# Performance work log

Measured on AMD Instinct MI355X. Metric: run time of the kernel, lower is better.

Reference implementation:

```python
import jax, jax.numpy as jnp
import numpy as np

HEADS = 16

def setup_inputs() -> dict:
    key = jax.random.key(0)
    k1, k2, k3 = jax.random.split(key, 3)
    B, T, C = 4, 2048, 1024
    s = 0.02
    return {
        "x": jax.random.normal(k1, (B, T, C), dtype=jnp.float32),
        "W_qkv": jax.random.normal(k2, (C, 3 * C), dtype=jnp.float32) * s,
        "b_qkv": jnp.zeros((3 * C,), dtype=jnp.float32),
        "W_pr": jax.random.normal(k3, (C, C), dtype=jnp.float32) * s,
        "b_pr": jnp.zeros((C,), dtype=jnp.float32),
    }

def reference(x, W_qkv, b_qkv, W_pr, b_pr):
    B, T, C = x.shape
    H = HEADS
    hd = C // H
    qkv = x @ W_qkv + b_qkv                     # [B,T,3C]
    q, k, v = jnp.split(qkv, 3, axis=-1)
    # [B,T,C] -> [B,H,T,hd]
    q = q.reshape(B, T, H, hd).transpose(0, 2, 1, 3)
    k = k.reshape(B, T, H, hd).transpose(0, 2, 1, 3)
    v = v.reshape(B, T, H, hd).transpose(0, 2, 1, 3)
    att = jnp.einsum('bhqd,bhkd->bhqk', q, k) * (1.0 / jnp.sqrt(jnp.float32(hd)))
    causal = jnp.tril(jnp.ones((T, T), dtype=bool))
    att = jnp.where(causal[None, None, :, :], att, jnp.float32(-jnp.inf))
    att = jax.nn.softmax(att, axis=-1)
    y = jnp.einsum('bhqk,bhkd->bhqd', att, v)   # [B,H,T,hd]
    y = y.transpose(0, 2, 1, 3).reshape(B, T, C)  # merge heads
    return y @ W_pr + b_pr
```

## Files before the change

kernel.cpp:

```cpp
#include <hip/hip_runtime.h>


typedef __attribute__((ext_vector_type(8))) short bf16x8;
typedef __attribute__((ext_vector_type(4))) float f32x4;

#define MFMA16(a, b, c) __builtin_amdgcn_mfma_f32_16x16x32_bf16(a, b, c, 0, 0, 0)

#define QK_SCALE 0.1803368801111244f

__device__ __forceinline__ unsigned short f2bf(float f) {
    union { float f; unsigned u; } v; v.f = f;
    unsigned r = v.u + 0x7fffu + ((v.u >> 16) & 1u);
    return (unsigned short)(r >> 16);
}

typedef __attribute__((address_space(1))) const unsigned int guint;
typedef __attribute__((address_space(3))) unsigned int luint;
__device__ __forceinline__ void gload16(const void* g, void* l) {
    __builtin_amdgcn_global_load_lds((guint*)g, (luint*)l, 16, 0, 0);
}

__device__ __forceinline__ float exp2_hw(float x) {
    float y;
    asm("v_exp_f32 %0, %1" : "=v"(y) : "v"(x));
    return y;
}

__device__ __forceinline__ unsigned cvt_pk_bf16(float lo, float hi) {
    unsigned w;
    asm("v_cvt_pk_bf16_f32 %0, %1, %2" : "=v"(w) : "v"(lo), "v"(hi));
    return w;
}

__global__ __launch_bounds__(256) void k_conv(const float* __restrict__ in,
                                              unsigned short* __restrict__ out,
                                              int n4) {
    int i = blockIdx.x * 256 + threadIdx.x;
    if (i >= n4) return;
    float4 v = reinterpret_cast<const float4*>(in)[i];
    ushort4 o;
    o.x = f2bf(v.x); o.y = f2bf(v.y); o.z = f2bf(v.z); o.w = f2bf(v.w);
    reinterpret_cast<ushort4*>(out)[i] = o;
}

__global__ __launch_bounds__(256) void k_transpose_conv(const float* __restrict__ W,
                                                        unsigned short* __restrict__ Wt,
                                                        int K, int N) {
    __shared__ unsigned short tile[32][33];
    int tx = threadIdx.x & 31, ty = threadIdx.x >> 5;
    int bn = blockIdx.x * 32, bk = blockIdx.y * 32;
#pragma unroll
    for (int i = 0; i < 32; i += 8)
        tile[ty + i][tx] = f2bf(W[(size_t)(bk + ty + i) * N + bn + tx]);
    __syncthreads();
#pragma unroll
    for (int i = 0; i < 32; i += 8)
        Wt[(size_t)(bn + ty + i) * K + bk + tx] = tile[tx][ty + i];
}

__device__ __forceinline__ int swz_src_col(int off) {
    return ((((off >> 4) & 3) ^ ((off >> 7) & 3)) << 3);
}

__global__ __launch_bounds__(256) void k_gemm_qkv(
    const unsigned short* __restrict__ A,
    const unsigned short* __restrict__ Bt,
    const float* __restrict__ bias,
    unsigned short* __restrict__ Qo,
    unsigned short* __restrict__ Ko,
    unsigned short* __restrict__ Vto)
{
    constexpr int K = 1024;
    __shared__ alignas(16) char smem[33280];
    unsigned short* Ep = (unsigned short*)smem;
    const int tid = threadIdx.x;
    const int wave = tid >> 6, lane = tid & 63;
    const int wr = wave >> 1, wc = wave & 1;
    const int lrow = lane & 15, lkg = lane >> 4;
    const int bm = blockIdx.y * 128, bn = blockIdx.x * 128;

    const int off0 = tid * 16, off1 = off0 + 4096;
    const unsigned short* gA0 = A + (size_t)(bm + (off0 >> 6)) * K + swz_src_col(off0);
    const unsigned short* gA1 = A + (size_t)(bm + (off1 >> 6)) * K + swz_src_col(off1);
    const unsigned short* gB0 = Bt + (size_t)(bn + (off0 >> 6)) * K + swz_src_col(off0);
    const unsigned short* gB1 = Bt + (size_t)(bn + (off1 >> 6)) * K + swz_src_col(off1);

    f32x4 acc[4][4] = {};

#define GSTAGE(kt_, bufn_)                                          \
    do {                                                            \
        char* ba_ = smem + (bufn_) * 16384;                         \
        gload16(gA0 + (kt_), ba_ + off0);                           \
        gload16(gA1 + (kt_), ba_ + off1);                           \
        gload16(gB0 + (kt_), ba_ + 8192 + off0);                    \
        gload16(gB1 + (kt_), ba_ + 8192 + off1);                    \
    } while (0)

    GSTAGE(0, 0);
    int buf = 0;
    for (int t = 0; t < 32; ++t) {
        if (t < 31) {
            GSTAGE((t + 1) * 32, buf ^ 1);
            asm volatile("s_waitcnt vmcnt(4)" ::: "memory");
        } else {
            asm volatile("s_waitcnt vmcnt(0)" ::: "memory");
        }
        __builtin_amdgcn_s_barrier();
        __builtin_amdgcn_sched_barrier(0);

        const char* Asb = smem + buf * 16384;
        const char* Bsb = Asb + 8192;
        bf16x8 af[4], bfr[4];
#pragma unroll
        for (int m = 0; m < 4; ++m) {
            int R = wr * 64 + m * 16 + lrow;
            af[m] = *reinterpret_cast<const bf16x8*>(
                Asb + R * 64 + ((lkg ^ ((R >> 1) & 3)) << 4));
        }
#pragma unroll
        for (int n = 0; n < 4; ++n) {
            int R = wc * 64 + n * 16 + lrow;
            bfr[n] = *reinterpret_cast<const bf16x8*>(
                Bsb + R * 64 + ((lkg ^ ((R >> 1) & 3)) << 4));
        }
        __builtin_amdgcn_s_setprio(1);
#pragma unroll
        for (int m = 0; m < 4; ++m)
#pragma unroll
            for (int n = 0; n < 4; ++n)
                acc[m][n] = MFMA16(af[m], bfr[n], acc[m][n]);
        __builtin_amdgcn_s_setprio(0);
        __builtin_amdgcn_s_barrier();
        buf ^= 1;
    }
#undef GSTAGE

    const int which = bn >> 10;
    const int h0 = (bn & 1023) >> 6;
    const int bq = bm >> 11;
    const int t0 = bm & 2047;
    const float qs = (which == 0) ? QK_SCALE : 1.0f;

#pragma unroll
    for (int m = 0; m < 4; ++m) {
        int rl = wr * 64 + m * 16 + lkg * 4;
#pragma unroll
        for (int n = 0; n < 4; ++n) {
            int cl = wc * 64 + n * 16 + lrow;
            float bia = bias[bn + cl];
#pragma unroll
            for (int r = 0; r < 4; ++r) {
                unsigned short val = f2bf((acc[m][n][r] + bia) * qs);
                if (which == 2) {
                    int tl = rl + r;
                    int pt = (tl & 0x60) | ((tl & 15) << 1) | ((tl >> 4) & 1);
                    Ep[cl * 130 + pt] = val;
                } else {
                    Ep[(rl + r) * 130 + cl] = val;
                }
            }
        }
    }
    __syncthreads();

    const int chunk = tid & 15, rbase = tid >> 4;
    if (which != 2) {
        const int head = chunk >> 3, d0 = (chunk & 7) * 8;
        unsigned short* dst = (which == 0 ? Qo : Ko) +
            (size_t)((bq * 16 + h0 + head) * 2048 + t0) * 64 + d0;
#pragma unroll
        for (int s = 0; s < 8; ++s) {
            int row = s * 16 + rbase;
            bf16x8 v = *reinterpret_cast<const bf16x8*>(&Ep[row * 130 + chunk * 8]);
            *reinterpret_cast<bf16x8*>(dst + (size_t)row * 64) = v;
        }
    } else {
#pragma unroll
        for (int s = 0; s < 8; ++s) {
            int pd = s * 16 + rbase;
            bf16x8 v = *reinterpret_cast<const bf16x8*>(&Ep[pd * 130 + chunk * 8]);
            int bh = bq * 16 + h0 + (pd >> 6);
            size_t addr = ((size_t)(bh * 64 + (pd & 63)) * 2048) + t0 + chunk * 8;
            *reinterpret_cast<bf16x8*>(Vto + addr) = v;
        }
    }
}

__global__ __launch_bounds__(256, 2) void k_attn(
    const unsigned short* __restrict__ Q,
    const unsigned short* __restrict__ Kg,
    const unsigned short* __restrict__ Vt,
    unsigned short* __restrict__ Y)
{
    __shared__ alignas(16) unsigned short Ks[2][4096];
    __shared__ alignas(16) unsigned short Vs[2][4096];
    __shared__ unsigned int Pu[4][32][36];
    const int tid = threadIdx.x;
    const int wave = tid >> 6, lane = tid & 63;
    const int lrow = lane & 15, lkg = lane >> 4;
    const int bh = blockIdx.x & 63;
    const int s = (blockIdx.x >> 6) & 3;
    const int band = blockIdx.x >> 8;
    const int j = (band == 0) ? 15 - s : (band == 1) ? 8 + s : (band == 2) ? 7 - s : s;
    const int qt = 4 * j + wave;
    const int q0 = qt * 32;
    const int nt = 2 * j + 2;
    const int b = bh >> 4, hh = bh & 15;

    const unsigned short* Qh = Q + (size_t)bh * 2048 * 64;
    const unsigned short* Kh = Kg + (size_t)bh * 2048 * 64;
    const unsigned short* Vh = Vt + (size_t)bh * 64 * 2048;

    const int srow = tid >> 3;
    const int swz = ((tid & 7) ^ (srow & 7)) << 3;
    const unsigned short* gK = Kh + (size_t)srow * 64 + swz;
    const unsigned short* gV = Vh + (size_t)srow * 2048 + swz;
    char* dK0 = (char*)&Ks[0][0] + tid * 16;
    char* dV0 = (char*)&Vs[0][0] + tid * 16;

    bf16x8 aq[2][2];
#pragma unroll
    for (int h = 0; h < 2; ++h)
#pragma unroll
        for (int ks = 0; ks < 2; ++ks)
            aq[h][ks] = *reinterpret_cast<const bf16x8*>(
                &Qh[(size_t)(q0 + h * 16 + lrow) * 64 + ks * 32 + lkg * 8]);

    f32x4 acc[2][4] = {};
    float lsum[2][4] = {};

#define STAGE(kb_, bufn_)                                           \
    do {                                                            \
        const unsigned short* k0_ = gK + (kb_) * 64;                \
        const unsigned short* v0_ = gV + (kb_);                     \
        char* dk_ = dK0 + (bufn_) * 8192;                           \
        char* dv_ = dV0 + (bufn_) * 8192;                           \
        gload16(k0_, dk_);                                          \
        gload16(k0_ + 2048, dk_ + 4096);                            \
        gload16(v0_, dv_);                                          \
        gload16(v0_ + 65536, dv_ + 4096);                           \
    } while (0)

    STAGE(0, 0);
    int buf = 0;

    for (int t = 0; t < nt; ++t) {
        if (t + 1 < nt) {
            STAGE((t + 1) * 64, buf ^ 1);
            asm volatile("s_waitcnt vmcnt(4)" ::: "memory");
        } else {
            asm volatile("s_waitcnt vmcnt(0)" ::: "memory");
        }
        __builtin_amdgcn_s_barrier();
        __builtin_amdgcn_sched_barrier(0);

        const int kb = t * 64;
        const char* kbase = (const char*)&Ks[buf][0];
        const char* vbase = (const char*)&Vs[buf][0];

        f32x4 s_[2][4] = {};
        __builtin_amdgcn_s_setprio(1);
#pragma unroll
        for (int sub = 0; sub < 4; ++sub) {
            int krow = sub * 16 + lrow;
            bf16x8 kf0 = *reinterpret_cast<const bf16x8*>(
                kbase + krow * 128 + ((lkg ^ (krow & 7)) << 4));
            bf16x8 kf1 = *reinterpret_cast<const bf16x8*>(
                kbase + krow * 128 + (((4 + lkg) ^ (krow & 7)) << 4));
            s_[0][sub] = MFMA16(aq[0][0], kf0, s_[0][sub]);
            s_[0][sub] = MFMA16(aq[0][1], kf1, s_[0][sub]);
            s_[1][sub] = MFMA16(aq[1][0], kf0, s_[1][sub]);
            s_[1][sub] = MFMA16(aq[1][1], kf1, s_[1][sub]);
        }
        __builtin_amdgcn_s_setprio(0);

        const bool need_mask = (kb + 64 > q0);
#pragma unroll
        for (int h = 0; h < 2; ++h)
#pragma unroll
            for (int sub = 0; sub < 4; ++sub)
#pragma unroll
                for (int r = 0; r < 4; ++r) {
                    float v = s_[h][sub][r];
                    if (need_mask) {
                        int key = kb + sub * 16 + lrow;
                        int q = q0 + h * 16 + lkg * 4 + r;
                        v = (key <= q) ? v : -1e30f;
                    }
                    s_[h][sub][r] = exp2_hw(v);
                }

#pragma unroll
        for (int h = 0; h < 2; ++h) {
            int prow = h * 16 + lkg * 4;
#pragma unroll
            for (int r = 0; r < 4; ++r) {
                lsum[h][r] += (s_[h][0][r] + s_[h][1][r]) + (s_[h][2][r] + s_[h][3][r]);
                Pu[wave][prow + r][lrow]      = cvt_pk_bf16(s_[h][0][r], s_[h][1][r]);
                Pu[wave][prow + r][16 + lrow] = cvt_pk_bf16(s_[h][2][r], s_[h][3][r]);
            }
        }

        bf16x8 pf[2][2];
#pragma unroll
        for (int h = 0; h < 2; ++h)
#pragma unroll
            for (int kc = 0; kc < 2; ++kc)
                pf[h][kc] = *reinterpret_cast<const bf16x8*>(
                    &Pu[wave][h * 16 + lrow][kc * 16 + lkg * 4]);

        __builtin_amdgcn_s_setprio(1);
#pragma unroll
        for (int tt = 0; tt < 4; ++tt) {
            int vrow = tt * 16 + lrow;
            bf16x8 vf0 = *reinterpret_cast<const bf16x8*>(
                vbase + vrow * 128 + ((lkg ^ (vrow & 7)) << 4));
            bf16x8 vf1 = *reinterpret_cast<const bf16x8*>(
                vbase + vrow * 128 + (((4 + lkg) ^ (vrow & 7)) << 4));
            acc[0][tt] = MFMA16(pf[0][0], vf0, acc[0][tt]);
            acc[0][tt] = MFMA16(pf[0][1], vf1, acc[0][tt]);
            acc[1][tt] = MFMA16(pf[1][0], vf0, acc[1][tt]);
            acc[1][tt] = MFMA16(pf[1][1], vf1, acc[1][tt]);
        }
        __builtin_amdgcn_s_setprio(0);

        __builtin_amdgcn_s_barrier();
        buf ^= 1;
    }
#undef STAGE

#pragma unroll
    for (int h = 0; h < 2; ++h) {
        float inv[4];
#pragma unroll
        for (int r = 0; r < 4; ++r) {
            float l = lsum[h][r];
            l += __shfl_xor(l, 1); l += __shfl_xor(l, 2);
            l += __shfl_xor(l, 4); l += __shfl_xor(l, 8);
            inv[r] = 1.0f / l;
        }
#pragma unroll
        for (int t = 0; t < 4; ++t)
#pragma unroll
            for (int r = 0; r < 4; ++r) {
                int q = q0 + h * 16 + lkg * 4 + r;
                size_t idx = ((size_t)b * 2048 + q) * 1024 + hh * 64 + t * 16 + lrow;
                Y[idx] = f2bf(acc[h][t][r] * inv[r]);
            }
    }
}

__global__ __launch_bounds__(256) void k_gemm_proj(
    const unsigned short* __restrict__ A,
    const unsigned short* __restrict__ Bt,
    const float* __restrict__ bias,
    float* __restrict__ out)
{
    constexpr int K = 1024;
    __shared__ alignas(16) char smem[33024];
    float* Ep2 = (float*)smem;
    const int tid = threadIdx.x;
    const int wave = tid >> 6, lane = tid & 63;
    const int wr = wave >> 1, wc = wave & 1;
    const int lrow = lane & 15, lkg = lane >> 4;
    const int bm = blockIdx.y * 128, bn = blockIdx.x * 128;

    const int off0 = tid * 16, off1 = off0 + 4096;
    const unsigned short* gA0 = A + (size_t)(bm + (off0 >> 6)) * K + swz_src_col(off0);
    const unsigned short* gA1 = A + (size_t)(bm + (off1 >> 6)) * K + swz_src_col(off1);
    const unsigned short* gB0 = Bt + (size_t)(bn + (off0 >> 6)) * K + swz_src_col(off0);
    const unsigned short* gB1 = Bt + (size_t)(bn + (off1 >> 6)) * K + swz_src_col(off1);

    f32x4 acc[4][4] = {};

#define GSTAGE(kt_, bufn_)                                          \
    do {                                                            \
        char* ba_ = smem + (bufn_) * 16384;                         \
        gload16(gA0 + (kt_), ba_ + off0);                           \
        gload16(gA1 + (kt_), ba_ + off1);                           \
        gload16(gB0 + (kt_), ba_ + 8192 + off0);                    \
        gload16(gB1 + (kt_), ba_ + 8192 + off1);                    \
    } while (0)

    GSTAGE(0, 0);
    int buf = 0;
    for (int t = 0; t < 32; ++t) {
        if (t < 31) {
            GSTAGE((t + 1) * 32, buf ^ 1);
            asm volatile("s_waitcnt vmcnt(4)" ::: "memory");
        } else {
            asm volatile("s_waitcnt vmcnt(0)" ::: "memory");
        }
        __builtin_amdgcn_s_barrier();
        __builtin_amdgcn_sched_barrier(0);

        const char* Asb = smem + buf * 16384;
        const char* Bsb = Asb + 8192;
        bf16x8 af[4], bfr[4];
#pragma unroll
        for (int m = 0; m < 4; ++m) {
            int R = wr * 64 + m * 16 + lrow;
            af[m] = *reinterpret_cast<const bf16x8*>(
                Asb + R * 64 + ((lkg ^ ((R >> 1) & 3)) << 4));
        }
#pragma unroll
        for (int n = 0; n < 4; ++n) {
            int R = wc * 64 + n * 16 + lrow;
            bfr[n] = *reinterpret_cast<const bf16x8*>(
                Bsb + R * 64 + ((lkg ^ ((R >> 1) & 3)) << 4));
        }
        __builtin_amdgcn_s_setprio(1);
#pragma unroll
        for (int m = 0; m < 4; ++m)
#pragma unroll
            for (int n = 0; n < 4; ++n)
                acc[m][n] = MFMA16(af[m], bfr[n], acc[m][n]);
        __builtin_amdgcn_s_setprio(0);
        __builtin_amdgcn_s_barrier();
        buf ^= 1;
    }
#undef GSTAGE

    const int chunk = tid >> 3;
    const int r8 = tid & 7;
#pragma unroll
    for (int p = 0; p < 2; ++p) {
        __syncthreads();
        if (wr == p) {
#pragma unroll
            for (int m = 0; m < 4; ++m)
#pragma unroll
                for (int n = 0; n < 4; ++n) {
                    int cl = wc * 64 + n * 16 + lrow;
                    float bia = bias[bn + cl];
#pragma unroll
                    for (int r = 0; r < 4; ++r)
                        Ep2[(m * 16 + lkg * 4 + r) * 129 + cl] = acc[m][n][r] + bia;
                }
        }
        __syncthreads();
#pragma unroll
        for (int s = 0; s < 8; ++s) {
            int row = r8 * 8 + s;
            float4 v = *reinterpret_cast<const float4*>(&Ep2[row * 129 + chunk * 4]);
            *reinterpret_cast<float4*>(&out[(size_t)(bm + p * 64 + row) * 1024 + bn + chunk * 4]) = v;
        }
    }
}

extern "C" void kernel_launch(void* const* d_in, const int* in_sizes, int n_in,
                              void* d_out, int out_size, void* d_ws, size_t ws_size,
                              hipStream_t stream) {
    const float* x    = (const float*)d_in[0];
    const float* Wqkv = (const float*)d_in[1];
    const float* bqkv = (const float*)d_in[2];
    const float* Wpr  = (const float*)d_in[3];
    const float* bpr  = (const float*)d_in[4];
    float* out = (float*)d_out;

    char* ws = (char*)d_ws;
    unsigned short* xb  = (unsigned short*)(ws);
    unsigned short* Wqt = (unsigned short*)(ws + 16777216);
    unsigned short* Wpt = (unsigned short*)(ws + 23068672);
    unsigned short* Qb  = (unsigned short*)(ws + 25165824);
    unsigned short* Kb  = (unsigned short*)(ws + 41943040);
    unsigned short* Vt  = (unsigned short*)(ws + 58720256);
    unsigned short* Y   = xb;

    k_conv<<<8192, 256, 0, stream>>>(x, xb, 8388608 / 4);
    k_transpose_conv<<<dim3(96, 32), 256, 0, stream>>>(Wqkv, Wqt, 1024, 3072);
    k_transpose_conv<<<dim3(32, 32), 256, 0, stream>>>(Wpr, Wpt, 1024, 1024);
    k_gemm_qkv<<<dim3(24, 64), 256, 0, stream>>>(xb, Wqt, bqkv, Qb, Kb, Vt);
    k_attn<<<1024, 256, 0, stream>>>(Qb, Kb, Vt, Y);
    k_gemm_proj<<<dim3(8, 64), 256, 0, stream>>>(Y, Wpt, bpr, out);
}
```

Baseline: 178.4 us.

## Enlarge GEMM tiles to 256x256 with 512 threads and triple-buffered LDS pipeline

Both the QKV and output-projection GEMMs move from 128x128 tiles with 4 waves to 256x256 tiles with 8 waves, each wave computing 128x64. The LDS staging ring grows from two to three buffers with a prefetch distance of two. The epilogues are split into row halves or quarters so the staging buffer fits in the enlarged shared memory. The aim is more operand reuse per byte loaded and better latency hiding. The cost is much larger LDS per block and far fewer blocks: 384 for QKV and 128 for projection, which may leave CUs idle or create tail imbalance.

```diff
diff --git a/kernel.cpp b/kernel.cpp
--- a/kernel.cpp
+++ b/kernel.cpp
@@ -62,7 +62,7 @@
     return ((((off >> 4) & 3) ^ ((off >> 7) & 3)) << 3);
 }
 
-__global__ __launch_bounds__(256) void k_gemm_qkv(
+__global__ __launch_bounds__(512, 2) void k_gemm_qkv(
     const unsigned short* __restrict__ A,
     const unsigned short* __restrict__ Bt,
     const float* __restrict__ bias,
@@ -71,36 +71,39 @@
     unsigned short* __restrict__ Vto)
 {
     constexpr int K = 1024;
-    __shared__ alignas(16) char smem[33280];
-    unsigned short* Ep = (unsigned short*)smem;
+    __shared__ alignas(16) char smem[98304];
     const int tid = threadIdx.x;
     const int wave = tid >> 6, lane = tid & 63;
-    const int wr = wave >> 1, wc = wave & 1;
+    const int wr = wave >> 2, wc = wave & 3;
     const int lrow = lane & 15, lkg = lane >> 4;
-    const int bm = blockIdx.y * 128, bn = blockIdx.x * 128;
-
-    const int off0 = tid * 16, off1 = off0 + 4096;
+    const int bm = blockIdx.y * 256, bn = blockIdx.x * 256;
+
+    const int off0 = tid * 16, off1 = off0 + 8192;
     const unsigned short* gA0 = A + (size_t)(bm + (off0 >> 6)) * K + swz_src_col(off0);
     const unsigned short* gA1 = A + (size_t)(bm + (off1 >> 6)) * K + swz_src_col(off1);
     const unsigned short* gB0 = Bt + (size_t)(bn + (off0 >> 6)) * K + swz_src_col(off0);
     const unsigned short* gB1 = Bt + (size_t)(bn + (off1 >> 6)) * K + swz_src_col(off1);
 
-    f32x4 acc[4][4] = {};
-
-#define GSTAGE(kt_, bufn_)                                          \
+    f32x4 acc[8][4] = {};
+
+#define GSTAGE(kt_, slot_)                                          \
     do {                                                            \
-        char* ba_ = smem + (bufn_) * 16384;                         \
-        gload16(gA0 + (kt_), ba_ + off0);                           \
-        gload16(gA1 + (kt_), ba_ + off1);                           \
-        gload16(gB0 + (kt_), ba_ + 8192 + off0);                    \
-        gload16(gB1 + (kt_), ba_ + 8192 + off1);                    \
+        char* base_ = smem + (slot_) * 32768;                       \
+        gload16(gA0 + (kt_), base_ + off0);                         \
+        gload16(gA1 + (kt_), base_ + off1);                         \
+        gload16(gB0 + (kt_), base_ + 16384 + off0);                 \
+        gload16(gB1 + (kt_), base_ + 16384 + off1);                 \
     } while (0)
 
     GSTAGE(0, 0);
-    int buf = 0;
+    GSTAGE(32, 1);
+    int cs = 0;
     for (int t = 0; t < 32; ++t) {
-        if (t < 31) {
-            GSTAGE((t + 1) * 32, buf ^ 1);
+        if (t < 30) {
+            int ns = cs + 2; if (ns >= 3) ns -= 3;
+            GSTAGE((t + 2) * 32, ns);
+            asm volatile("s_waitcnt vmcnt(8)" ::: "memory");
+        } else if (t == 30) {
             asm volatile("s_waitcnt vmcnt(4)" ::: "memory");
         } else {
             asm volatile("s_waitcnt vmcnt(0)" ::: "memory");
@@ -108,30 +111,30 @@
         __builtin_amdgcn_s_barrier();
         __builtin_amdgcn_sched_barrier(0);
 
-        const char* Asb = smem + buf * 16384;
-        const char* Bsb = Asb + 8192;
-        bf16x8 af[4], bfr[4];
-#pragma unroll
-        for (int m = 0; m < 4; ++m) {
-            int R = wr * 64 + m * 16 + lrow;
+        const char* Ab = smem + cs * 32768;
+        const char* Bb = Ab + 16384;
+        bf16x8 af[8], bfr[4];
+#pragma unroll
+        for (int m = 0; m < 8; ++m) {
+            int R = wr * 128 + m * 16 + lrow;
             af[m] = *reinterpret_cast<const bf16x8*>(
-                Asb + R * 64 + ((lkg ^ ((R >> 1) & 3)) << 4));
+                Ab + R * 64 + ((lkg ^ ((R >> 1) & 3)) << 4));
         }
 #pragma unroll
         for (int n = 0; n < 4; ++n) {
             int R = wc * 64 + n * 16 + lrow;
             bfr[n] = *reinterpret_cast<const bf16x8*>(
-                Bsb + R * 64 + ((lkg ^ ((R >> 1) & 3)) << 4));
+                Bb + R * 64 + ((lkg ^ ((R >> 1) & 3)) << 4));
         }
         __builtin_amdgcn_s_setprio(1);
 #pragma unroll
-        for (int m = 0; m < 4; ++m)
+        for (int m = 0; m < 8; ++m)
 #pragma unroll
             for (int n = 0; n < 4; ++n)
                 acc[m][n] = MFMA16(af[m], bfr[n], acc[m][n]);
         __builtin_amdgcn_s_setprio(0);
         __builtin_amdgcn_s_barrier();
-        buf ^= 1;
+        ++cs; if (cs == 3) cs = 0;
     }
 #undef GSTAGE
 
@@ -140,48 +143,55 @@
     const int bq = bm >> 11;
     const int t0 = bm & 2047;
     const float qs = (which == 0) ? QK_SCALE : 1.0f;
-
-#pragma unroll
-    for (int m = 0; m < 4; ++m) {
-        int rl = wr * 64 + m * 16 + lkg * 4;
-#pragma unroll
-        for (int n = 0; n < 4; ++n) {
-            int cl = wc * 64 + n * 16 + lrow;
-            float bia = bias[bn + cl];
-#pragma unroll
-            for (int r = 0; r < 4; ++r) {
-                unsigned short val = f2bf((acc[m][n][r] + bia) * qs);
-                if (which == 2) {
-                    int tl = rl + r;
-                    int pt = (tl & 0x60) | ((tl & 15) << 1) | ((tl >> 4) & 1);
-                    Ep[cl * 130 + pt] = val;
-                } else {
-                    Ep[(rl + r) * 130 + cl] = val;
+    unsigned short* Ep = (unsigned short*)smem;
+
+#pragma unroll
+    for (int p = 0; p < 2; ++p) {
+        __syncthreads();
+        if (wr == p) {
+#pragma unroll
+            for (int m = 0; m < 8; ++m) {
+                int tl = m * 16 + lkg * 4;
+#pragma unroll
+                for (int n = 0; n < 4; ++n) {
+                    int cl = wc * 64 + n * 16 + lrow;
+                    float bia = bias[bn + cl];
+#pragma unroll
+                    for (int r = 0; r < 4; ++r) {
+                        unsigned short val = f2bf((acc[m][n][r] + bia) * qs);
+                        int trow = tl + r;
+                        if (which == 2) {
+                            int pt = (trow & 0x60) | ((trow & 15) << 1) | ((trow >> 4) & 1);
+                            Ep[cl * 130 + pt] = val;
+                        } else {
+                            Ep[trow * 258 + cl] = val;
+                        }
+                    }
                 }
             }
         }
-    }
-    __syncthreads();
-
-    const int chunk = tid & 15, rbase = tid >> 4;
-    if (which != 2) {
-        const int head = chunk >> 3, d0 = (chunk & 7) * 8;
-        unsigned short* dst = (which == 0 ? Qo : Ko) +
-            (size_t)((bq * 16 + h0 + head) * 2048 + t0) * 64 + d0;
-#pragma unroll
-        for (int s = 0; s < 8; ++s) {
-            int row = s * 16 + rbase;
-            bf16x8 v = *reinterpret_cast<const bf16x8*>(&Ep[row * 130 + chunk * 8]);
-            *reinterpret_cast<bf16x8*>(dst + (size_t)row * 64) = v;
-        }
-    } else {
-#pragma unroll
-        for (int s = 0; s < 8; ++s) {
-            int pd = s * 16 + rbase;
-            bf16x8 v = *reinterpret_cast<const bf16x8*>(&Ep[pd * 130 + chunk * 8]);
-            int bh = bq * 16 + h0 + (pd >> 6);
-            size_t addr = ((size_t)(bh * 64 + (pd & 63)) * 2048) + t0 + chunk * 8;
-            *reinterpret_cast<bf16x8*>(Vto + addr) = v;
+        __syncthreads();
+        if (which != 2) {
+            const int chunk = tid & 31, rbase = tid >> 5;
+            const int head = h0 + (chunk >> 3), d0 = (chunk & 7) * 8;
+            unsigned short* dst = (which == 0 ? Qo : Ko) +
+                (size_t)((bq * 16 + head) * 2048 + t0 + p * 128) * 64 + d0;
+#pragma unroll
+            for (int s = 0; s < 8; ++s) {
+                int row = s * 16 + rbase;
+                bf16x8 v = *reinterpret_cast<const bf16x8*>(&Ep[row * 258 + chunk * 8]);
+                *reinterpret_cast<bf16x8*>(dst + (size_t)row * 64) = v;
+            }
+        } else {
+            const int chunkt = tid & 15, crow = tid >> 4;
+#pragma unroll
+            for (int s = 0; s < 8; ++s) {
+                int cl = s * 32 + crow;
+                bf16x8 v = *reinterpret_cast<const bf16x8*>(&Ep[cl * 130 + chunkt * 8]);
+                int bh = bq * 16 + h0 + (cl >> 6);
+                size_t addr = ((size_t)(bh * 64 + (cl & 63)) * 2048) + t0 + p * 128 + chunkt * 8;
+                *reinterpret_cast<bf16x8*>(Vto + addr) = v;
+            }
         }
     }
 }
@@ -350,43 +360,46 @@
     }
 }
 
-__global__ __launch_bounds__(256) void k_gemm_proj(
+__global__ __launch_bounds__(512, 2) void k_gemm_proj(
     const unsigned short* __restrict__ A,
     const unsigned short* __restrict__ Bt,
     const float* __restrict__ bias,
     float* __restrict__ out)
 {
     constexpr int K = 1024;
-    __shared__ alignas(16) char smem[33024];
-    float* Ep2 = (float*)smem;
+    __shared__ alignas(16) char smem[98304];
     const int tid = threadIdx.x;
     const int wave = tid >> 6, lane = tid & 63;
-    const int wr = wave >> 1, wc = wave & 1;
+    const int wr = wave >> 2, wc = wave & 3;
     const int lrow = lane & 15, lkg = lane >> 4;
-    const int bm = blockIdx.y * 128, bn = blockIdx.x * 128;
-
-    const int off0 = tid * 16, off1 = off0 + 4096;
+    const int bm = blockIdx.y * 256, bn = blockIdx.x * 256;
+
+    const int off0 = tid * 16, off1 = off0 + 8192;
     const unsigned short* gA0 = A + (size_t)(bm + (off0 >> 6)) * K + swz_src_col(off0);
     const unsigned short* gA1 = A + (size_t)(bm + (off1 >> 6)) * K + swz_src_col(off1);
     const unsigned short* gB0 = Bt + (size_t)(bn + (off0 >> 6)) * K + swz_src_col(off0);
     const unsigned short* gB1 = Bt + (size_t)(bn + (off1 >> 6)) * K + swz_src_col(off1);
 
-    f32x4 acc[4][4] = {};
-
-#define GSTAGE(kt_, bufn_)                                          \
+    f32x4 acc[8][4] = {};
+
+#define GSTAGE(kt_, slot_)                                          \
     do {                                                            \
-        char* ba_ = smem + (bufn_) * 16384;                         \
-        gload16(gA0 + (kt_), ba_ + off0);                           \
-        gload16(gA1 + (kt_), ba_ + off1);                           \
-        gload16(gB0 + (kt_), ba_ + 8192 + off0);                    \
-        gload16(gB1 + (kt_), ba_ + 8192 + off1);                    \
+        char* base_ = smem + (slot_) * 32768;                       \
+        gload16(gA0 + (kt_), base_ + off0);                         \
+        gload16(gA1 + (kt_), base_ + off1);                         \
+        gload16(gB0 + (kt_), base_ + 16384 + off0);                 \
+        gload16(gB1 + (kt_), base_ + 16384 + off1);                 \
     } while (0)
 
     GSTAGE(0, 0);
-    int buf = 0;
+    GSTAGE(32, 1);
+    int cs = 0;
     for (int t = 0; t < 32; ++t) {
-        if (t < 31) {
-            GSTAGE((t + 1) * 32, buf ^ 1);
+        if (t < 30) {
+            int ns = cs + 2; if (ns >= 3) ns -= 3;
+            GSTAGE((t + 2) * 32, ns);
+            asm volatile("s_waitcnt vmcnt(8)" ::: "memory");
+        } else if (t == 30) {
             asm volatile("s_waitcnt vmcnt(4)" ::: "memory");
         } else {
             asm volatile("s_waitcnt vmcnt(0)" ::: "memory");
@@ -394,56 +407,61 @@
         __builtin_amdgcn_s_barrier();
         __builtin_amdgcn_sched_barrier(0);
 
-        const char* Asb = smem + buf * 16384;
-        const char* Bsb = Asb + 8192;
-        bf16x8 af[4], bfr[4];
-#pragma unroll
-        for (int m = 0; m < 4; ++m) {
-            int R = wr * 64 + m * 16 + lrow;
+        const char* Ab = smem + cs * 32768;
+        const char* Bb = Ab + 16384;
+        bf16x8 af[8], bfr[4];
+#pragma unroll
+        for (int m = 0; m < 8; ++m) {
+            int R = wr * 128 + m * 16 + lrow;
             af[m] = *reinterpret_cast<const bf16x8*>(
-                Asb + R * 64 + ((lkg ^ ((R >> 1) & 3)) << 4));
+                Ab + R * 64 + ((lkg ^ ((R >> 1) & 3)) << 4));
         }
 #pragma unroll
         for (int n = 0; n < 4; ++n) {
             int R = wc * 64 + n * 16 + lrow;
             bfr[n] = *reinterpret_cast<const bf16x8*>(
-                Bsb + R * 64 + ((lkg ^ ((R >> 1) & 3)) << 4));
+                Bb + R * 64 + ((lkg ^ ((R >> 1) & 3)) << 4));
         }
         __builtin_amdgcn_s_setprio(1);
 #pragma unroll
-        for (int m = 0; m < 4; ++m)
+        for (int m = 0; m < 8; ++m)
 #pragma unroll
             for (int n = 0; n < 4; ++n)
                 acc[m][n] = MFMA16(af[m], bfr[n], acc[m][n]);
         __builtin_amdgcn_s_setprio(0);
         __builtin_amdgcn_s_barrier();
-        buf ^= 1;
+        ++cs; if (cs == 3) cs = 0;
     }
 #undef GSTAGE
 
-    const int chunk = tid >> 3;
-    const int r8 = tid & 7;
-#pragma unroll
-    for (int p = 0; p < 2; ++p) {
+    float* Ep2 = (float*)smem;
+#pragma unroll
+    for (int p = 0; p < 4; ++p) {
         __syncthreads();
-        if (wr == p) {
-#pragma unroll
-            for (int m = 0; m < 4; ++m)
+        if (wr == (p >> 1)) {
+            int mbase = (p & 1) * 4;
+#pragma unroll
+            for (int mm = 0; mm < 4; ++mm) {
+                int m = mbase + mm;
+                int rl = mm * 16 + lkg * 4;
 #pragma unroll
                 for (int n = 0; n < 4; ++n) {
                     int cl = wc * 64 + n * 16 + lrow;
                     float bia = bias[bn + cl];
 #pragma unroll
                     for (int r = 0; r < 4; ++r)
-                        Ep2[(m * 16 + lkg * 4 + r) * 129 + cl] = acc[m][n][r] + bia;
+                        Ep2[(rl + r) * 257 + cl] = acc[m][n][r] + bia;
                 }
+            }
         }
         __syncthreads();
+        const int chunk = tid & 63, rbase = tid >> 6;
 #pragma unroll
         for (int s = 0; s < 8; ++s) {
-            int row = r8 * 8 + s;
-            float4 v = *reinterpret_cast<const float4*>(&Ep2[row * 129 + chunk * 4]);
-            *reinterpret_cast<float4*>(&out[(size_t)(bm + p * 64 + row) * 1024 + bn + chunk * 4]) = v;
+            int row = s * 8 + rbase;
+            float4 v = *reinterpret_cast<const float4*>(&Ep2[row * 257 + chunk * 4]);
+            *reinterpret_cast<float4*>(
+                &out[(size_t)(bm + p * 64 + row) * 1024 + bn + chunk * 4]) = v;
         }
     }
 }
@@ -470,7 +488,7 @@
     k_conv<<<8192, 256, 0, stream>>>(x, xb, 8388608 / 4);
     k_transpose_conv<<<dim3(96, 32), 256, 0, stream>>>(Wqkv, Wqt, 1024, 3072);
     k_transpose_conv<<<dim3(32, 32), 256, 0, stream>>>(Wpr, Wpt, 1024, 1024);
-    k_gemm_qkv<<<dim3(24, 64), 256, 0, stream>>>(xb, Wqt, bqkv, Qb, Kb, Vt);
+    k_gemm_qkv<<<dim3(12, 32), 512, 0, stream>>>(xb, Wqt, bqkv, Qb, Kb, Vt);
     k_attn<<<1024, 256, 0, stream>>>(Qb, Kb, Vt, Y);
-    k_gemm_proj<<<dim3(8, 64), 256, 0, stream>>>(Y, Wpt, bpr, out);
-}
+    k_gemm_proj<<<dim3(4, 32), 512, 0, stream>>>(Y, Wpt, bpr, out);
+}
```

Result: slower. 208.7 us (+16.9%).

## Enlarge QKV GEMM tile to 256x128 and fuse prep conversions into one launch

Applied to the files above, without the earlier changes.

The QKV projection GEMM now computes 256x128 output tiles (8x4 MFMA accumulators per wave) instead of 128x128, halving the grid and reusing each B tile across twice as many rows. The epilogue is staged through shared memory in two halves to fit the LDS budget. The x conversion and both weight transpose-conversions are merged into a single k_prep launch to cut launch overhead. The larger tile raises register pressure (launch_bounds 256,2) and leaves fewer blocks (768) to fill the CUs.

```diff
diff --git a/kernel.cpp b/kernel.cpp
--- a/kernel.cpp
+++ b/kernel.cpp
@@ -32,23 +32,26 @@
     return w;
 }
 
-__global__ __launch_bounds__(256) void k_conv(const float* __restrict__ in,
-                                              unsigned short* __restrict__ out,
-                                              int n4) {
-    int i = blockIdx.x * 256 + threadIdx.x;
-    if (i >= n4) return;
-    float4 v = reinterpret_cast<const float4*>(in)[i];
-    ushort4 o;
-    o.x = f2bf(v.x); o.y = f2bf(v.y); o.z = f2bf(v.z); o.w = f2bf(v.w);
-    reinterpret_cast<ushort4*>(out)[i] = o;
-}
-
-__global__ __launch_bounds__(256) void k_transpose_conv(const float* __restrict__ W,
-                                                        unsigned short* __restrict__ Wt,
-                                                        int K, int N) {
+__global__ __launch_bounds__(256) void k_prep(
+    const float* __restrict__ x, unsigned short* __restrict__ xb,
+    const float* __restrict__ Wqkv, unsigned short* __restrict__ Wqt,
+    const float* __restrict__ Wpr, unsigned short* __restrict__ Wpt) {
     __shared__ unsigned short tile[32][33];
+    const int b = blockIdx.x;
+    if (b < 8192) {
+        int i = b * 256 + threadIdx.x;
+        float4 v = reinterpret_cast<const float4*>(x)[i];
+        ushort4 o;
+        o.x = f2bf(v.x); o.y = f2bf(v.y); o.z = f2bf(v.z); o.w = f2bf(v.w);
+        reinterpret_cast<ushort4*>(xb)[i] = o;
+        return;
+    }
+    const float* W; unsigned short* Wt; int K, N, idx;
+    if (b < 11264) { W = Wqkv; Wt = Wqt; K = 1024; N = 3072; idx = b - 8192;  }
+    else           { W = Wpr;  Wt = Wpt; K = 1024; N = 1024; idx = b - 11264; }
+    const int nb = N / 32;
+    const int bn = (idx % nb) * 32, bk = (idx / nb) * 32;
     int tx = threadIdx.x & 31, ty = threadIdx.x >> 5;
-    int bn = blockIdx.x * 32, bk = blockIdx.y * 32;
 #pragma unroll
     for (int i = 0; i < 32; i += 8)
         tile[ty + i][tx] = f2bf(W[(size_t)(bk + ty + i) * N + bn + tx]);
@@ -62,7 +65,7 @@
     return ((((off >> 4) & 3) ^ ((off >> 7) & 3)) << 3);
 }
 
-__global__ __launch_bounds__(256) void k_gemm_qkv(
+__global__ __launch_bounds__(256, 2) void k_gemm_qkv(
     const unsigned short* __restrict__ A,
     const unsigned short* __restrict__ Bt,
     const float* __restrict__ bias,
@@ -71,29 +74,37 @@
     unsigned short* __restrict__ Vto)
 {
     constexpr int K = 1024;
-    __shared__ alignas(16) char smem[33280];
-    unsigned short* Ep = (unsigned short*)smem;
+    __shared__ alignas(16) char smem[49152];
     const int tid = threadIdx.x;
     const int wave = tid >> 6, lane = tid & 63;
     const int wr = wave >> 1, wc = wave & 1;
     const int lrow = lane & 15, lkg = lane >> 4;
-    const int bm = blockIdx.y * 128, bn = blockIdx.x * 128;
-
-    const int off0 = tid * 16, off1 = off0 + 4096;
-    const unsigned short* gA0 = A + (size_t)(bm + (off0 >> 6)) * K + swz_src_col(off0);
-    const unsigned short* gA1 = A + (size_t)(bm + (off1 >> 6)) * K + swz_src_col(off1);
-    const unsigned short* gB0 = Bt + (size_t)(bn + (off0 >> 6)) * K + swz_src_col(off0);
-    const unsigned short* gB1 = Bt + (size_t)(bn + (off1 >> 6)) * K + swz_src_col(off1);
-
-    f32x4 acc[4][4] = {};
-
-#define GSTAGE(kt_, bufn_)                                          \
+    const int bm = blockIdx.y * 256, bn = blockIdx.x * 128;
+
+    const unsigned short* gA[4];
+    const unsigned short* gB[2];
+#pragma unroll
+    for (int i = 0; i < 4; ++i) {
+        int off = tid * 16 + i * 4096;
+        gA[i] = A + (size_t)(bm + (off >> 6)) * K + swz_src_col(off);
+    }
+#pragma unroll
+    for (int i = 0; i < 2; ++i) {
+        int off = tid * 16 + i * 4096;
+        gB[i] = Bt + (size_t)(bn + (off >> 6)) * K + swz_src_col(off);
+    }
+
+    f32x4 acc[8][4] = {};
+
+#define GSTAGE(kt_, slot_)                                          \
     do {                                                            \
-        char* ba_ = smem + (bufn_) * 16384;                         \
-        gload16(gA0 + (kt_), ba_ + off0);                           \
-        gload16(gA1 + (kt_), ba_ + off1);                           \
-        gload16(gB0 + (kt_), ba_ + 8192 + off0);                    \
-        gload16(gB1 + (kt_), ba_ + 8192 + off1);                    \
+        char* base_ = smem + (slot_) * 24576;                       \
+        gload16(gA[0] + (kt_), base_ + tid * 16);                   \
+        gload16(gA[1] + (kt_), base_ + 4096 + tid * 16);            \
+        gload16(gA[2] + (kt_), base_ + 8192 + tid * 16);            \
+        gload16(gA[3] + (kt_), base_ + 12288 + tid * 16);           \
+        gload16(gB[0] + (kt_), base_ + 16384 + tid * 16);           \
+        gload16(gB[1] + (kt_), base_ + 20480 + tid * 16);           \
     } while (0)
 
     GSTAGE(0, 0);
@@ -101,31 +112,31 @@
     for (int t = 0; t < 32; ++t) {
         if (t < 31) {
             GSTAGE((t + 1) * 32, buf ^ 1);
-            asm volatile("s_waitcnt vmcnt(4)" ::: "memory");
+            asm volatile("s_waitcnt vmcnt(6)" ::: "memory");
         } else {
             asm volatile("s_waitcnt vmcnt(0)" ::: "memory");
         }
         __builtin_amdgcn_s_barrier();
         __builtin_amdgcn_sched_barrier(0);
 
-        const char* Asb = smem + buf * 16384;
-        const char* Bsb = Asb + 8192;
-        bf16x8 af[4], bfr[4];
-#pragma unroll
-        for (int m = 0; m < 4; ++m) {
-            int R = wr * 64 + m * 16 + lrow;
+        const char* Ab = smem + buf * 24576;
+        const char* Bb = Ab + 16384;
+        bf16x8 af[8], bfr[4];
+#pragma unroll
+        for (int m = 0; m < 8; ++m) {
+            int R = wr * 128 + m * 16 + lrow;
             af[m] = *reinterpret_cast<const bf16x8*>(
-                Asb + R * 64 + ((lkg ^ ((R >> 1) & 3)) << 4));
+                Ab + R * 64 + ((lkg ^ ((R >> 1) & 3)) << 4));
         }
 #pragma unroll
         for (int n = 0; n < 4; ++n) {
             int R = wc * 64 + n * 16 + lrow;
             bfr[n] = *reinterpret_cast<const bf16x8*>(
-                Bsb + R * 64 + ((lkg ^ ((R >> 1) & 3)) << 4));
+                Bb + R * 64 + ((lkg ^ ((R >> 1) & 3)) << 4));
         }
         __builtin_amdgcn_s_setprio(1);
 #pragma unroll
-        for (int m = 0; m < 4; ++m)
+        for (int m = 0; m < 8; ++m)
 #pragma unroll
             for (int n = 0; n < 4; ++n)
                 acc[m][n] = MFMA16(af[m], bfr[n], acc[m][n]);
@@ -140,48 +151,55 @@
     const int bq = bm >> 11;
     const int t0 = bm & 2047;
     const float qs = (which == 0) ? QK_SCALE : 1.0f;
-
-#pragma unroll
-    for (int m = 0; m < 4; ++m) {
-        int rl = wr * 64 + m * 16 + lkg * 4;
-#pragma unroll
-        for (int n = 0; n < 4; ++n) {
-            int cl = wc * 64 + n * 16 + lrow;
-            float bia = bias[bn + cl];
-#pragma unroll
-            for (int r = 0; r < 4; ++r) {
-                unsigned short val = f2bf((acc[m][n][r] + bia) * qs);
-                if (which == 2) {
-                    int tl = rl + r;
-                    int pt = (tl & 0x60) | ((tl & 15) << 1) | ((tl >> 4) & 1);
-                    Ep[cl * 130 + pt] = val;
-                } else {
-                    Ep[(rl + r) * 130 + cl] = val;
+    unsigned short* Ep = (unsigned short*)smem;
+
+#pragma unroll
+    for (int p = 0; p < 2; ++p) {
+        __syncthreads();
+        if (wr == p) {
+#pragma unroll
+            for (int m = 0; m < 8; ++m) {
+                int tl = m * 16 + lkg * 4;
+#pragma unroll
+                for (int n = 0; n < 4; ++n) {
+                    int cl = wc * 64 + n * 16 + lrow;
+                    float bia = bias[bn + cl];
+#pragma unroll
+                    for (int r = 0; r < 4; ++r) {
+                        unsigned short val = f2bf((acc[m][n][r] + bia) * qs);
+                        int trow = tl + r;
+                        if (which == 2) {
+                            int pt = (trow & 0x60) | ((trow & 15) << 1) | ((trow >> 4) & 1);
+                            Ep[cl * 130 + pt] = val;
+                        } else {
+                            Ep[trow * 130 + cl] = val;
+                        }
+                    }
                 }
             }
         }
-    }
-    __syncthreads();
-
-    const int chunk = tid & 15, rbase = tid >> 4;
-    if (which != 2) {
-        const int head = chunk >> 3, d0 = (chunk & 7) * 8;
-        unsigned short* dst = (which == 0 ? Qo : Ko) +
-            (size_t)((bq * 16 + h0 + head) * 2048 + t0) * 64 + d0;
-#pragma unroll
-        for (int s = 0; s < 8; ++s) {
-            int row = s * 16 + rbase;
-            bf16x8 v = *reinterpret_cast<const bf16x8*>(&Ep[row * 130 + chunk * 8]);
-            *reinterpret_cast<bf16x8*>(dst + (size_t)row * 64) = v;
-        }
-    } else {
-#pragma unroll
-        for (int s = 0; s < 8; ++s) {
-            int pd = s * 16 + rbase;
-            bf16x8 v = *reinterpret_cast<const bf16x8*>(&Ep[pd * 130 + chunk * 8]);
-            int bh = bq * 16 + h0 + (pd >> 6);
-            size_t addr = ((size_t)(bh * 64 + (pd & 63)) * 2048) + t0 + chunk * 8;
-            *reinterpret_cast<bf16x8*>(Vto + addr) = v;
+        __syncthreads();
+        if (which != 2) {
+            const int chunk = tid & 15, rbase = tid >> 4;
+            const int head = h0 + (chunk >> 3), d0 = (chunk & 7) * 8;
+            unsigned short* dst = (which == 0 ? Qo : Ko) +
+                (size_t)((bq * 16 + head) * 2048 + t0 + p * 128) * 64 + d0;
+#pragma unroll
+            for (int s = 0; s < 8; ++s) {
+                int row = s * 16 + rbase;
+                bf16x8 v = *reinterpret_cast<const bf16x8*>(&Ep[row * 130 + chunk * 8]);
+                *reinterpret_cast<bf16x8*>(dst + (size_t)row * 64) = v;
+            }
+        } else {
+            const int chunkt = tid & 15, crow = tid >> 4;
+#pragma unroll
+            for (int s = 0; s < 8; ++s) {
+                int cl = s * 16 + crow;
+                bf16x8 v = *reinterpret_cast<const bf16x8*>(&Ep[cl * 130 + chunkt * 8]);
+                int bh = bq * 16 + h0 + (cl >> 6);
+                size_t addr = ((size_t)(bh * 64 + (cl & 63)) * 2048) + t0 + p * 128 + chunkt * 8;
+                *reinterpret_cast<bf16x8*>(Vto + addr) = v;
+            }
         }
     }
 }
@@ -467,10 +485,8 @@
     unsigned short* Vt  = (unsigned short*)(ws + 58720256);
     unsigned short* Y   = xb;
 
-    k_conv<<<8192, 256, 0, stream>>>(x, xb, 8388608 / 4);
-    k_transpose_conv<<<dim3(96, 32), 256, 0, stream>>>(Wqkv, Wqt, 1024, 3072);
-    k_transpose_conv<<<dim3(32, 32), 256, 0, stream>>>(Wpr, Wpt, 1024, 1024);
-    k_gemm_qkv<<<dim3(24, 64), 256, 0, stream>>>(xb, Wqt, bqkv, Qb, Kb, Vt);
+    k_prep<<<12288, 256, 0, stream>>>(x, xb, Wqkv, Wqt, Wpr, Wpt);
+    k_gemm_qkv<<<dim3(24, 32), 256, 0, stream>>>(xb, Wqt, bqkv, Qb, Kb, Vt);
     k_attn<<<1024, 256, 0, stream>>>(Qb, Kb, Vt, Y);
     k_gemm_proj<<<dim3(8, 64), 256, 0, stream>>>(Y, Wpt, bpr, out);
 }
```

Result: slower. 185.5 us (+4.0%).

## Fuse prep kernels and deepen GEMM K-tile to 64 with new swizzle

Applied to the files above, without the earlier changes.

Merges the x conversion and the two weight transpose-conversion kernels into a single launch that dispatches on block index, removing two launches. Both GEMMs now stage 64-wide K tiles (64KB double-buffered LDS) with an 8-way XOR swizzle, halving the number of barrier iterations and doubling the MFMAs per sync. The pipeline now waits vmcnt(0) and issues the next prefetch after the barrier, and the trailing barrier is dropped. The larger LDS footprint limits occupancy, and prefetch overlap is shallower since the loads are issued only after the wait.

```diff
diff --git a/kernel.cpp b/kernel.cpp
--- a/kernel.cpp
+++ b/kernel.cpp
@@ -32,23 +32,26 @@
     return w;
 }
 
-__global__ __launch_bounds__(256) void k_conv(const float* __restrict__ in,
-                                              unsigned short* __restrict__ out,
-                                              int n4) {
-    int i = blockIdx.x * 256 + threadIdx.x;
-    if (i >= n4) return;
-    float4 v = reinterpret_cast<const float4*>(in)[i];
-    ushort4 o;
-    o.x = f2bf(v.x); o.y = f2bf(v.y); o.z = f2bf(v.z); o.w = f2bf(v.w);
-    reinterpret_cast<ushort4*>(out)[i] = o;
-}
-
-__global__ __launch_bounds__(256) void k_transpose_conv(const float* __restrict__ W,
-                                                        unsigned short* __restrict__ Wt,
-                                                        int K, int N) {
+__global__ __launch_bounds__(256) void k_prep(
+    const float* __restrict__ x, unsigned short* __restrict__ xb,
+    const float* __restrict__ Wqkv, unsigned short* __restrict__ Wqt,
+    const float* __restrict__ Wpr, unsigned short* __restrict__ Wpt) {
     __shared__ unsigned short tile[32][33];
+    const int b = blockIdx.x;
+    if (b < 8192) {
+        int i = b * 256 + threadIdx.x;
+        float4 v = reinterpret_cast<const float4*>(x)[i];
+        ushort4 o;
+        o.x = f2bf(v.x); o.y = f2bf(v.y); o.z = f2bf(v.z); o.w = f2bf(v.w);
+        reinterpret_cast<ushort4*>(xb)[i] = o;
+        return;
+    }
+    const float* W; unsigned short* Wt; int K, N, idx;
+    if (b < 11264) { W = Wqkv; Wt = Wqt; K = 1024; N = 3072; idx = b - 8192;  }
+    else           { W = Wpr;  Wt = Wpt; K = 1024; N = 1024; idx = b - 11264; }
+    const int nb = N / 32;
+    const int bn = (idx % nb) * 32, bk = (idx / nb) * 32;
     int tx = threadIdx.x & 31, ty = threadIdx.x >> 5;
-    int bn = blockIdx.x * 32, bk = blockIdx.y * 32;
 #pragma unroll
     for (int i = 0; i < 32; i += 8)
         tile[ty + i][tx] = f2bf(W[(size_t)(bk + ty + i) * N + bn + tx]);
@@ -58,11 +61,8 @@
         Wt[(size_t)(bn + ty + i) * K + bk + tx] = tile[tx][ty + i];
 }
 
-__device__ __forceinline__ int swz_src_col(int off) {
-    return ((((off >> 4) & 3) ^ ((off >> 7) & 3)) << 3);
-}
-
-__global__ __launch_bounds__(256) void k_gemm_qkv(
+
+__global__ __launch_bounds__(256, 2) void k_gemm_qkv(
     const unsigned short* __restrict__ A,
     const unsigned short* __restrict__ Bt,
     const float* __restrict__ bias,
@@ -71,7 +71,7 @@
     unsigned short* __restrict__ Vto)
 {
     constexpr int K = 1024;
-    __shared__ alignas(16) char smem[33280];
+    __shared__ alignas(16) char smem[65536];
     unsigned short* Ep = (unsigned short*)smem;
     const int tid = threadIdx.x;
     const int wave = tid >> 6, lane = tid & 63;
@@ -79,61 +79,71 @@
     const int lrow = lane & 15, lkg = lane >> 4;
     const int bm = blockIdx.y * 128, bn = blockIdx.x * 128;
 
-    const int off0 = tid * 16, off1 = off0 + 4096;
-    const unsigned short* gA0 = A + (size_t)(bm + (off0 >> 6)) * K + swz_src_col(off0);
-    const unsigned short* gA1 = A + (size_t)(bm + (off1 >> 6)) * K + swz_src_col(off1);
-    const unsigned short* gB0 = Bt + (size_t)(bn + (off0 >> 6)) * K + swz_src_col(off0);
-    const unsigned short* gB1 = Bt + (size_t)(bn + (off1 >> 6)) * K + swz_src_col(off1);
+    const int scol = (((tid & 7) ^ ((tid >> 3) & 7)) << 3);
+    const int r0 = tid >> 3;
+    const unsigned short* gA[4];
+    const unsigned short* gB[4];
+#pragma unroll
+    for (int i = 0; i < 4; ++i) {
+        gA[i] = A + (size_t)(bm + i * 32 + r0) * K + scol;
+        gB[i] = Bt + (size_t)(bn + i * 32 + r0) * K + scol;
+    }
 
     f32x4 acc[4][4] = {};
 
 #define GSTAGE(kt_, bufn_)                                          \
     do {                                                            \
-        char* ba_ = smem + (bufn_) * 16384;                         \
-        gload16(gA0 + (kt_), ba_ + off0);                           \
-        gload16(gA1 + (kt_), ba_ + off1);                           \
-        gload16(gB0 + (kt_), ba_ + 8192 + off0);                    \
-        gload16(gB1 + (kt_), ba_ + 8192 + off1);                    \
+        char* ba_ = smem + (bufn_) * 32768;                         \
+        gload16(gA[0] + (kt_), ba_ + tid * 16);                     \
+        gload16(gA[1] + (kt_), ba_ + 4096 + tid * 16);              \
+        gload16(gA[2] + (kt_), ba_ + 8192 + tid * 16);              \
+        gload16(gA[3] + (kt_), ba_ + 12288 + tid * 16);             \
+        gload16(gB[0] + (kt_), ba_ + 16384 + tid * 16);             \
+        gload16(gB[1] + (kt_), ba_ + 20480 + tid * 16);             \
+        gload16(gB[2] + (kt_), ba_ + 24576 + tid * 16);             \
+        gload16(gB[3] + (kt_), ba_ + 28672 + tid * 16);             \
     } while (0)
 
     GSTAGE(0, 0);
     int buf = 0;
-    for (int t = 0; t < 32; ++t) {
-        if (t < 31) {
-            GSTAGE((t + 1) * 32, buf ^ 1);
-            asm volatile("s_waitcnt vmcnt(4)" ::: "memory");
-        } else {
-            asm volatile("s_waitcnt vmcnt(0)" ::: "memory");
-        }
+    for (int t = 0; t < 16; ++t) {
+        asm volatile("s_waitcnt vmcnt(0)" ::: "memory");
         __builtin_amdgcn_s_barrier();
         __builtin_amdgcn_sched_barrier(0);
-
-        const char* Asb = smem + buf * 16384;
-        const char* Bsb = Asb + 8192;
-        bf16x8 af[4], bfr[4];
+        if (t < 15) GSTAGE((t + 1) * 64, buf ^ 1);
+
+        const char* Ab = smem + buf * 32768;
+        const char* Bb = Ab + 16384;
+        bf16x8 af[4][2], bfr[4][2];
 #pragma unroll
         for (int m = 0; m < 4; ++m) {
             int R = wr * 64 + m * 16 + lrow;
-            af[m] = *reinterpret_cast<const bf16x8*>(
-                Asb + R * 64 + ((lkg ^ ((R >> 1) & 3)) << 4));
+#pragma unroll
+            for (int k = 0; k < 2; ++k)
+                af[m][k] = *reinterpret_cast<const bf16x8*>(
+                    Ab + R * 128 + (((k * 4 + lkg) ^ (R & 7)) << 4));
         }
 #pragma unroll
         for (int n = 0; n < 4; ++n) {
             int R = wc * 64 + n * 16 + lrow;
-            bfr[n] = *reinterpret_cast<const bf16x8*>(
-                Bsb + R * 64 + ((lkg ^ ((R >> 1) & 3)) << 4));
+#pragma unroll
+            for (int k = 0; k < 2; ++k)
+                bfr[n][k] = *reinterpret_cast<const bf16x8*>(
+                    Bb + R * 128 + (((k * 4 + lkg) ^ (R & 7)) << 4));
         }
         __builtin_amdgcn_s_setprio(1);
 #pragma unroll
         for (int m = 0; m < 4; ++m)
 #pragma unroll
-            for (int n = 0; n < 4; ++n)
-                acc[m][n] = MFMA16(af[m], bfr[n], acc[m][n]);
+            for (int n = 0; n < 4; ++n) {
+                acc[m][n] = MFMA16(af[m][0], bfr[n][0], acc[m][n]);
+                acc[m][n] = MFMA16(af[m][1], bfr[n][1], acc[m][n]);
+            }
         __builtin_amdgcn_s_setprio(0);
-        __builtin_amdgcn_s_barrier();
         buf ^= 1;
     }
 #undef GSTAGE
+    __syncthreads();
 
     const int which = bn >> 10;
     const int h0 = (bn & 1023) >> 6;
@@ -350,14 +360,14 @@
     }
 }
 
-__global__ __launch_bounds__(256) void k_gemm_proj(
+__global__ __launch_bounds__(256, 2) void k_gemm_proj(
     const unsigned short* __restrict__ A,
     const unsigned short* __restrict__ Bt,
     const float* __restrict__ bias,
     float* __restrict__ out)
 {
     constexpr int K = 1024;
-    __shared__ alignas(16) char smem[33024];
+    __shared__ alignas(16) char smem[65536];
     float* Ep2 = (float*)smem;
     const int tid = threadIdx.x;
     const int wave = tid >> 6, lane = tid & 63;
@@ -365,58 +375,67 @@
     const int lrow = lane & 15, lkg = lane >> 4;
     const int bm = blockIdx.y * 128, bn = blockIdx.x * 128;
 
-    const int off0 = tid * 16, off1 = off0 + 4096;
-    const unsigned short* gA0 = A + (size_t)(bm + (off0 >> 6)) * K + swz_src_col(off0);
-    const unsigned short* gA1 = A + (size_t)(bm + (off1 >> 6)) * K + swz_src_col(off1);
-    const unsigned short* gB0 = Bt + (size_t)(bn + (off0 >> 6)) * K + swz_src_col(off0);
-    const unsigned short* gB1 = Bt + (size_t)(bn + (off1 >> 6)) * K + swz_src_col(off1);
+    const int scol = (((tid & 7) ^ ((tid >> 3) & 7)) << 3);
+    const int r0 = tid >> 3;
+    const unsigned short* gA[4];
+    const unsigned short* gB[4];
+#pragma unroll
+    for (int i = 0; i < 4; ++i) {
+        gA[i] = A + (size_t)(bm + i * 32 + r0) * K + scol;
+        gB[i] = Bt + (size_t)(bn + i * 32 + r0) * K + scol;
+    }
 
     f32x4 acc[4][4] = {};
 
 #define GSTAGE(kt_, bufn_)                                          \
     do {                                                            \
-        char* ba_ = smem + (bufn_) * 16384;                         \
-        gload16(gA0 + (kt_), ba_ + off0);                           \
-        gload16(gA1 + (kt_), ba_ + off1);                           \
-        gload16(gB0 + (kt_), ba_ + 8192 + off0);                    \
-        gload16(gB1 + (kt_), ba_ + 8192 + off1);                    \
+        char* ba_ = smem + (bufn_) * 32768;                         \
+        gload16(gA[0] + (kt_), ba_ + tid * 16);                     \
+        gload16(gA[1] + (kt_), ba_ + 4096 + tid * 16);              \
+        gload16(gA[2] + (kt_), ba_ + 8192 + tid * 16);              \
+        gload16(gA[3] + (kt_), ba_ + 12288 + tid * 16);             \
+        gload16(gB[0] + (kt_), ba_ + 16384 + tid * 16);             \
+        gload16(gB[1] + (kt_), ba_ + 20480 + tid * 16);             \
+        gload16(gB[2] + (kt_), ba_ + 24576 + tid * 16);             \
+        gload16(gB[3] + (kt_), ba_ + 28672 + tid * 16);             \
     } while (0)
 
     GSTAGE(0, 0);
     int buf = 0;
-    for (int t = 0; t < 32; ++t) {
-        if (t < 31) {
-            GSTAGE((t + 1) * 32, buf ^ 1);
-            asm volatile("s_waitcnt vmcnt(4)" ::: "memory");
-        } else {
-            asm volatile("s_waitcnt vmcnt(0)" ::: "memory");
-        }
+    for (int t = 0; t < 16; ++t) {
+        asm volatile("s_waitcnt vmcnt(0)" ::: "memory");
         __builtin_amdgcn_s_barrier();
         __builtin_amdgcn_sched_barrier(0);
-
-        const char* Asb = smem + buf * 16384;
-        const char* Bsb = Asb + 8192;
-        bf16x8 af[4], bfr[4];
+        if (t < 15) GSTAGE((t + 1) * 64, buf ^ 1);
+
+        const char* Ab = smem + buf * 32768;
+        const char* Bb = Ab + 16384;
+        bf16x8 af[4][2], bfr[4][2];
 #pragma unroll
         for (int m = 0; m < 4; ++m) {
             int R = wr * 64 + m * 16 + lrow;
-            af[m] = *reinterpret_cast<const bf16x8*>(
-                Asb + R * 64 + ((lkg ^ ((R >> 1) & 3)) << 4));
+#pragma unroll
+            for (int k = 0; k < 2; ++k)
+                af[m][k] = *reinterpret_cast<const bf16x8*>(
+                    Ab + R * 128 + (((k * 4 + lkg) ^ (R & 7)) << 4));
         }
 #pragma unroll
         for (int n = 0; n < 4; ++n) {
             int R = wc * 64 + n * 16 + lrow;
-            bfr[n] = *reinterpret_cast<const bf16x8*>(
-                Bsb + R * 64 + ((lkg ^ ((R >> 1) & 3)) << 4));
+#pragma unroll
+            for (int k = 0; k < 2; ++k)
+                bfr[n][k] = *reinterpret_cast<const bf16x8*>(
+                    Bb + R * 128 + (((k * 4 + lkg) ^ (R & 7)) << 4));
         }
         __builtin_amdgcn_s_setprio(1);
 #pragma unroll
         for (int m = 0; m < 4; ++m)
 #pragma unroll
-            for (int n = 0; n < 4; ++n)
-                acc[m][n] = MFMA16(af[m], bfr[n], acc[m][n]);
+            for (int n = 0; n < 4; ++n) {
+                acc[m][n] = MFMA16(af[m][0], bfr[n][0], acc[m][n]);
+                acc[m][n] = MFMA16(af[m][1], bfr[n][1], acc[m][n]);
+            }
         __builtin_amdgcn_s_setprio(0);
-        __builtin_amdgcn_s_barrier();
         buf ^= 1;
     }
 #undef GSTAGE
@@ -467,9 +486,7 @@
     unsigned short* Vt  = (unsigned short*)(ws + 58720256);
     unsigned short* Y   = xb;
 
-    k_conv<<<8192, 256, 0, stream>>>(x, xb, 8388608 / 4);
-    k_transpose_conv<<<dim3(96, 32), 256, 0, stream>>>(Wqkv, Wqt, 1024, 3072);
-    k_transpose_conv<<<dim3(32, 32), 256, 0, stream>>>(Wpr, Wpt, 1024, 1024);
+    k_prep<<<12288, 256, 0, stream>>>(x, xb, Wqkv, Wqt, Wpr, Wpt);
     k_gemm_qkv<<<dim3(24, 64), 256, 0, stream>>>(xb, Wqt, bqkv, Qb, Kb, Vt);
     k_attn<<<1024, 256, 0, stream>>>(Qb, Kb, Vt, Y);
     k_gemm_proj<<<dim3(8, 64), 256, 0, stream>>>(Y, Wpt, bpr, out);
```

After: 173.6 us. 2.7% less time.
